# Kernel tuning notes

Hardware: AMD Instinct MI355X
Metric: run time of the kernel (lower is better)

## Reference

```python
import jax, jax.numpy as jnp
import numpy as np

EPS = 1e-12  # matches torch F.normalize eps


def _gradients(img):
    # forward differences along D, H, W with last slice zeroed (via zero-pad)
    dx = jnp.pad(img[:, :, 1:] - img[:, :, :-1], ((0, 0), (0, 0), (0, 1), (0, 0), (0, 0)))
    dy = jnp.pad(img[:, :, :, 1:] - img[:, :, :, :-1], ((0, 0), (0, 0), (0, 0), (0, 1), (0, 0)))
    dz = jnp.pad(img[:, :, :, :, 1:] - img[:, :, :, :, :-1], ((0, 0), (0, 0), (0, 0), (0, 0), (0, 1)))
    return dx, dy, dz


def _cos(f, t, axis):
    # cosine similarity along `axis` with torch-normalize eps semantics
    fn = f / jnp.maximum(jnp.linalg.norm(f, axis=axis, keepdims=True), EPS)
    tn = t / jnp.maximum(jnp.linalg.norm(t, axis=axis, keepdims=True), EPS)
    return jnp.sum(fn * tn, axis=axis)


def _sploss(f, t, ax_row, ax_col):
    # trace(norm_rows(F) @ norm_rows(T)^T) == sum of row cosine sims; same for cols.
    bc = f.shape[0] * f.shape[1]
    a = jnp.sum(_cos(f, t, ax_col)) / (f.shape[ax_row] * bc)
    b = jnp.sum(_cos(f, t, ax_row)) / (f.shape[ax_col] * bc)
    return -(a + b)


def setup_inputs() -> dict:
    key = jax.random.key(0)
    k1, k2 = jax.random.split(key)
    shape = (2, 1, 160, 160, 160)  # [B, C, D, H, W]
    fake = jax.random.normal(k1, shape, dtype=jnp.float32)
    true = jax.random.normal(k2, shape, dtype=jnp.float32)
    return {"fake": fake, "true": true}


def reference(fake, true):
    fx, fy, fz = _gradients(fake)
    tx, ty, tz = _gradients(true)
    # dim='x' slices are [H, W] -> rows axis 3, cols axis 4
    trace_x = _sploss(fx, tx, 3, 4)
    # dim='y' slices are [D, W] -> rows axis 2, cols axis 4
    trace_y = _sploss(fy, ty, 2, 4)
    # dim='z' slices are [D, H] -> rows axis 2, cols axis 3
    trace_z = _sploss(fz, tz, 2, 3)
    return (trace_x + trace_y + trace_z) / 3.0
```

## Files before the change

kernel.cpp:

```cpp
#include <hip/hip_runtime.h>
#include <math.h>

#define DD 160
#define HH 160
#define WW 160
#define NB 2
#define SLICE (HH * WW)
#define NV 51200
#define Dt 4
#define NDC 40
#define NHC 10
#define HCS 16
#define NTHR 320

static constexpr float EPS = 1e-12f;
static constexpr float SCALE = -1.0f / 960.0f;

#define ELEM(v, j) ((j) == 0 ? (v).x : ((j) == 1 ? (v).y : ((j) == 2 ? (v).z : (v).w)))

__global__ void zero_kernel(float* out) {
  if (threadIdx.x == 0) out[0] = 0.0f;
}

__global__ __launch_bounds__(NTHR, 2) void mainS(const float* __restrict__ f,
                                                 const float* __restrict__ t,
                                                 float* __restrict__ P,
                                                 float* __restrict__ out) {
  __shared__ float sw[HCS * 40 * 7];
  __shared__ float sh[8 * 40 * 25];
  __shared__ float red[HCS][6];
  __shared__ float cpad[HCS];
  const int tid = threadIdx.x;
  const int g = tid / 40;
  const int l = tid % 40;
  const int w = 4 * l;
  const int wn = (w + 4 < WW) ? (w + 4) : (WW - 1);
  const int hc = blockIdx.x % NHC;
  const int t2 = blockIdx.x / NHC;
  const int dc = t2 % NDC;
  const int b  = t2 / NDC;
  const int d0 = dc * Dt;
  const int r0 = hc * HCS + g * 2;
  const int r1 = r0 + 1;
  const int r2 = (r1 + 1 < HH) ? (r1 + 1) : (HH - 1);
  const float* fb = f + (size_t)b * DD * SLICE;
  const float* tb = t + (size_t)b * DD * SLICE;
  float* pH = P;
  float* pD = P + (size_t)NHC * 6 * NV;

  float4 S0f = *(const float4*)(fb + (size_t)d0 * SLICE + r0 * WW + w);
  float4 S0t = *(const float4*)(tb + (size_t)d0 * SLICE + r0 * WW + w);
  float4 S1f = *(const float4*)(fb + (size_t)d0 * SLICE + r1 * WW + w);
  float4 S1t = *(const float4*)(tb + (size_t)d0 * SLICE + r1 * WW + w);
  float s0fz = (fb + (size_t)d0 * SLICE + r0 * WW)[wn];
  float s0tz = (tb + (size_t)d0 * SLICE + r0 * WW)[wn];
  float s1fz = (fb + (size_t)d0 * SLICE + r1 * WW)[wn];
  float s1tz = (tb + (size_t)d0 * SLICE + r1 * WW)[wn];

  float aD[48];
#pragma unroll
  for (int c = 0; c < 48; ++c) aD[c] = 0.0f;
  float accCos = 0.0f;

#pragma unroll
  for (int p = 0; p < Dt; ++p) {
    const int d = d0 + p;
    const int dn = (d + 1 < DD) ? (d + 1) : d;
    const float* fS = fb + (size_t)d * SLICE;
    const float* tS = tb + (size_t)d * SLICE;
    const float* fN = fb + (size_t)dn * SLICE;
    const float* tN = tb + (size_t)dn * SLICE;
    const float4 Hf  = *(const float4*)(fS + r2 * WW + w);
    const float4 Ht  = *(const float4*)(tS + r2 * WW + w);
    const float4 D0f = *(const float4*)(fN + r0 * WW + w);
    const float4 D0t = *(const float4*)(tN + r0 * WW + w);
    const float4 D1f = *(const float4*)(fN + r1 * WW + w);
    const float4 D1t = *(const float4*)(tN + r1 * WW + w);
    const float d0fz = (fN + r0 * WW)[wn], d0tz = (tN + r0 * WW)[wn];
    const float d1fz = (fN + r1 * WW)[wn], d1tz = (tN + r1 * WW)[wn];

    float aH[24];
#pragma unroll
    for (int c = 0; c < 24; ++c) aH[c] = 0.0f;

    {
      float xd = 0, xf = 0, xt = 0, yd = 0, yf = 0, yt = 0;
#pragma unroll
      for (int j = 0; j < 4; ++j) {
        const float f0 = ELEM(S0f, j), t0 = ELEM(S0t, j);
        const float gxf = ELEM(D0f, j) - f0, gxt = ELEM(D0t, j) - t0;
        const float gyf = ELEM(S1f, j) - f0, gyt = ELEM(S1t, j) - t0;
        const float fnx = (j < 3) ? ELEM(S0f, j + 1) : s0fz;
        const float tnx = (j < 3) ? ELEM(S0t, j + 1) : s0tz;
        const float gzf = fnx - f0, gzt = tnx - t0;
        xd += gxf * gxt; xf += gxf * gxf; xt += gxt * gxt;
        yd += gyf * gyt; yf += gyf * gyf; yt += gyt * gyt;
        aH[j * 6 + 0] += gxf * gxt; aH[j * 6 + 1] += gxf * gxf; aH[j * 6 + 2] += gxt * gxt;
        aH[j * 6 + 3] += gzf * gzt; aH[j * 6 + 4] += gzf * gzf; aH[j * 6 + 5] += gzt * gzt;
        aD[j * 6 + 0] += gyf * gyt; aD[j * 6 + 1] += gyf * gyf; aD[j * 6 + 2] += gyt * gyt;
        aD[j * 6 + 3] += gzf * gzt; aD[j * 6 + 4] += gzf * gzf; aD[j * 6 + 5] += gzt * gzt;
      }
      float* s = &sw[((g * 2 + 0) * 40 + l) * 7];
      s[0] = xd; s[1] = xf; s[2] = xt; s[3] = yd; s[4] = yf; s[5] = yt;
    }
    {
      float xd = 0, xf = 0, xt = 0, yd = 0, yf = 0, yt = 0;
#pragma unroll
      for (int j = 0; j < 4; ++j) {
        const float f0 = ELEM(S1f, j), t0 = ELEM(S1t, j);
        const float gxf = ELEM(D1f, j) - f0, gxt = ELEM(D1t, j) - t0;
        const float gyf = ELEM(Hf, j) - f0, gyt = ELEM(Ht, j) - t0;
        const float fnx = (j < 3) ? ELEM(S1f, j + 1) : s1fz;
        const float tnx = (j < 3) ? ELEM(S1t, j + 1) : s1tz;
        const float gzf = fnx - f0, gzt = tnx - t0;
        xd += gxf * gxt; xf += gxf * gxf; xt += gxt * gxt;
        yd += gyf * gyt; yf += gyf * gyf; yt += gyt * gyt;
        aH[j * 6 + 0] += gxf * gxt; aH[j * 6 + 1] += gxf * gxf; aH[j * 6 + 2] += gxt * gxt;
        aH[j * 6 + 3] += gzf * gzt; aH[j * 6 + 4] += gzf * gzf; aH[j * 6 + 5] += gzt * gzt;
        aD[(4 + j) * 6 + 0] += gyf * gyt; aD[(4 + j) * 6 + 1] += gyf * gyf; aD[(4 + j) * 6 + 2] += gyt * gyt;
        aD[(4 + j) * 6 + 3] += gzf * gzt; aD[(4 + j) * 6 + 4] += gzf * gzf; aD[(4 + j) * 6 + 5] += gzt * gzt;
      }
      float* s = &sw[((g * 2 + 1) * 40 + l) * 7];
      s[0] = xd; s[1] = xf; s[2] = xt; s[3] = yd; s[4] = yf; s[5] = yt;
    }
    {
      float* s2 = &sh[(g * 40 + l) * 25];
#pragma unroll
      for (int c = 0; c < 24; ++c) s2[c] = aH[c];
    }
    S0f = D0f; S0t = D0t; S1f = D1f; S1t = D1t;
    s0fz = d0fz; s0tz = d0tz; s1fz = d1fz; s1tz = d1tz;
    __syncthreads();

    if (tid < 240) {
      const int cc = tid / 40, ll = tid % 40;
      float v0 = 0, v1 = 0, v2 = 0, v3 = 0;
#pragma unroll
      for (int gg = 0; gg < 8; ++gg) {
        const float* q = &sh[(gg * 40 + ll) * 25];
        v0 += q[0 * 6 + cc]; v1 += q[1 * 6 + cc]; v2 += q[2 * 6 + cc]; v3 += q[3 * 6 + cc];
      }
      const int bd = b * DD + d;
      float4 o; o.x = v0; o.y = v1; o.z = v2; o.w = v3;
      *(float4*)(pH + ((size_t)(hc * 6 + cc)) * NV + bd * 160 + 4 * ll) = o;
    } else {
      for (int k = tid - 240; k < HCS * 6; k += 80) {
        const int row = k / 6, c = k % 6;
        float s = 0.0f;
#pragma unroll 8
        for (int ll = 0; ll < 40; ++ll) s += sw[(row * 40 + ll) * 7 + c];
        red[row][c] = s;
      }
    }
    __syncthreads();
    if (tid < HCS) {
      const float cx = red[tid][0] / (fmaxf(sqrtf(red[tid][1]), EPS) * fmaxf(sqrtf(red[tid][2]), EPS));
      const float cy = red[tid][3] / (fmaxf(sqrtf(red[tid][4]), EPS) * fmaxf(sqrtf(red[tid][5]), EPS));
      accCos += cx + cy;
    }
  }

#pragma unroll
  for (int r = 0; r < 2; ++r) {
    const int h = r0 + r;
#pragma unroll
    for (int cc = 0; cc < 6; ++cc) {
      float4 o;
      o.x = aD[(r * 4 + 0) * 6 + cc];
      o.y = aD[(r * 4 + 1) * 6 + cc];
      o.z = aD[(r * 4 + 2) * 6 + cc];
      o.w = aD[(r * 4 + 3) * 6 + cc];
      *(float4*)(pD + ((size_t)(dc * 6 + cc)) * NV + b * SLICE + h * 160 + 4 * l) = o;
    }
  }

  if (tid < HCS) cpad[tid] = accCos;
  __syncthreads();
  if (tid == 0) {
    float s = 0.0f;
#pragma unroll
    for (int i = 0; i < HCS; ++i) s += cpad[i];
    atomicAdd(out, s * SCALE);
  }
}

__global__ __launch_bounds__(256) void finalize_kernel(const float* __restrict__ P,
                                                       float* __restrict__ out) {
  const int v = blockIdx.x * 256 + threadIdx.x;
  float c = 0.0f;
  if (v < 4 * NV) {
    const int type = v / NV;
    const int vec = v % NV;
    float dot = 0.0f, ff = 0.0f, tt = 0.0f;
    if (type < 2) {
#pragma unroll
      for (int ch = 0; ch < NHC; ++ch) {
        const float* q = P + ((size_t)(ch * 6 + type * 3)) * NV + vec;
        dot += q[0]; ff += q[(size_t)NV]; tt += q[2 * (size_t)NV];
      }
    } else {
      const float* pD = P + (size_t)NHC * 6 * NV;
#pragma unroll 8
      for (int ch = 0; ch < NDC; ++ch) {
        const float* q = pD + ((size_t)(ch * 6 + (type - 2) * 3)) * NV + vec;
        dot += q[0]; ff += q[(size_t)NV]; tt += q[2 * (size_t)NV];
      }
    }
    c = dot / (fmaxf(sqrtf(ff), EPS) * fmaxf(sqrtf(tt), EPS));
  }
#pragma unroll
  for (int m = 32; m >= 1; m >>= 1) c += __shfl_xor(c, m);
  __shared__ float part[4];
  if ((threadIdx.x & 63) == 0) part[threadIdx.x >> 6] = c;
  __syncthreads();
  if (threadIdx.x == 0) atomicAdd(out, (part[0] + part[1] + part[2] + part[3]) * SCALE);
}

extern "C" void kernel_launch(void* const* d_in, const int* in_sizes, int n_in,
                              void* d_out, int out_size, void* d_ws, size_t ws_size,
                              hipStream_t stream) {
  const float* fk = (const float*)d_in[0];
  const float* tr = (const float*)d_in[1];
  float* out = (float*)d_out;
  float* P = (float*)d_ws;

  hipLaunchKernelGGL(zero_kernel, dim3(1), dim3(64), 0, stream, out);
  hipLaunchKernelGGL(mainS, dim3(NB * NDC * NHC), dim3(NTHR), 0, stream, fk, tr, P, out);
  hipLaunchKernelGGL(finalize_kernel, dim3((4 * NV + 255) / 256), dim3(256), 0, stream, P, out);
}
```

Baseline: 145.8 us.

## Split D-axis partial sums into separate kernel to shrink partial buffer

Moves the per-(b,h,w) D-direction partial accumulation out of the main kernel into a new gradD kernel that sums over D in only four chunks. The partial buffer for the y/z cosines therefore drops from 40 chunks to 4, which cuts the workspace writes and the finalize reads. It also software-prefetches the next D slice in the main kernel. The cost is a second full read of both inputs and an extra kernel launch.

```diff
diff --git a/kernel.cpp b/kernel.cpp
--- a/kernel.cpp
+++ b/kernel.cpp
@@ -12,6 +12,8 @@
 #define NHC 10
 #define HCS 16
 #define NTHR 320
+#define DQ 4
+#define DPG 5
 
 static constexpr float EPS = 1e-12f;
 static constexpr float SCALE = -1.0f / 960.0f;
@@ -22,9 +24,9 @@
   if (threadIdx.x == 0) out[0] = 0.0f;
 }
 
-__global__ __launch_bounds__(NTHR, 2) void mainS(const float* __restrict__ f,
+__global__ __launch_bounds__(NTHR, 2) void gradH(const float* __restrict__ f,
                                                  const float* __restrict__ t,
-                                                 float* __restrict__ P,
+                                                 float* __restrict__ pH,
                                                  float* __restrict__ out) {
   __shared__ float sw[HCS * 40 * 7];
   __shared__ float sh[8 * 40 * 25];
@@ -45,8 +47,6 @@
   const int r2 = (r1 + 1 < HH) ? (r1 + 1) : (HH - 1);
   const float* fb = f + (size_t)b * DD * SLICE;
   const float* tb = t + (size_t)b * DD * SLICE;
-  float* pH = P;
-  float* pD = P + (size_t)NHC * 6 * NV;
 
   float4 S0f = *(const float4*)(fb + (size_t)d0 * SLICE + r0 * WW + w);
   float4 S0t = *(const float4*)(tb + (size_t)d0 * SLICE + r0 * WW + w);
@@ -56,28 +56,39 @@
   float s0tz = (tb + (size_t)d0 * SLICE + r0 * WW)[wn];
   float s1fz = (fb + (size_t)d0 * SLICE + r1 * WW)[wn];
   float s1tz = (tb + (size_t)d0 * SLICE + r1 * WW)[wn];
-
-  float aD[48];
-#pragma unroll
-  for (int c = 0; c < 48; ++c) aD[c] = 0.0f;
+  const float* fN0 = fb + (size_t)(d0 + 1) * SLICE;
+  const float* tN0 = tb + (size_t)(d0 + 1) * SLICE;
+  float4 D0f = *(const float4*)(fN0 + r0 * WW + w);
+  float4 D0t = *(const float4*)(tN0 + r0 * WW + w);
+  float4 D1f = *(const float4*)(fN0 + r1 * WW + w);
+  float4 D1t = *(const float4*)(tN0 + r1 * WW + w);
+  float d0fz = (fN0 + r0 * WW)[wn], d0tz = (tN0 + r0 * WW)[wn];
+  float d1fz = (fN0 + r1 * WW)[wn], d1tz = (tN0 + r1 * WW)[wn];
+
   float accCos = 0.0f;
 
 #pragma unroll
   for (int p = 0; p < Dt; ++p) {
     const int d = d0 + p;
-    const int dn = (d + 1 < DD) ? (d + 1) : d;
     const float* fS = fb + (size_t)d * SLICE;
     const float* tS = tb + (size_t)d * SLICE;
-    const float* fN = fb + (size_t)dn * SLICE;
-    const float* tN = tb + (size_t)dn * SLICE;
-    const float4 Hf  = *(const float4*)(fS + r2 * WW + w);
-    const float4 Ht  = *(const float4*)(tS + r2 * WW + w);
-    const float4 D0f = *(const float4*)(fN + r0 * WW + w);
-    const float4 D0t = *(const float4*)(tN + r0 * WW + w);
-    const float4 D1f = *(const float4*)(fN + r1 * WW + w);
-    const float4 D1t = *(const float4*)(tN + r1 * WW + w);
-    const float d0fz = (fN + r0 * WW)[wn], d0tz = (tN + r0 * WW)[wn];
-    const float d1fz = (fN + r1 * WW)[wn], d1tz = (tN + r1 * WW)[wn];
+    const float4 Hf = *(const float4*)(fS + r2 * WW + w);
+    const float4 Ht = *(const float4*)(tS + r2 * WW + w);
+    float4 nD0f = {0, 0, 0, 0}, nD0t = {0, 0, 0, 0};
+    float4 nD1f = {0, 0, 0, 0}, nD1t = {0, 0, 0, 0};
+    float n0fz = 0.f, n0tz = 0.f, n1fz = 0.f, n1tz = 0.f;
+    if (p < Dt - 1) {
+      const int nd = d + 1;
+      const int ndn = (nd + 1 < DD) ? (nd + 1) : nd;
+      const float* fN = fb + (size_t)ndn * SLICE;
+      const float* tN = tb + (size_t)ndn * SLICE;
+      nD0f = *(const float4*)(fN + r0 * WW + w);
+      nD0t = *(const float4*)(tN + r0 * WW + w);
+      nD1f = *(const float4*)(fN + r1 * WW + w);
+      nD1t = *(const float4*)(tN + r1 * WW + w);
+      n0fz = (fN + r0 * WW)[wn]; n0tz = (tN + r0 * WW)[wn];
+      n1fz = (fN + r1 * WW)[wn]; n1tz = (tN + r1 * WW)[wn];
+    }
 
     float aH[24];
 #pragma unroll
@@ -97,8 +108,6 @@
         yd += gyf * gyt; yf += gyf * gyf; yt += gyt * gyt;
         aH[j * 6 + 0] += gxf * gxt; aH[j * 6 + 1] += gxf * gxf; aH[j * 6 + 2] += gxt * gxt;
         aH[j * 6 + 3] += gzf * gzt; aH[j * 6 + 4] += gzf * gzf; aH[j * 6 + 5] += gzt * gzt;
-        aD[j * 6 + 0] += gyf * gyt; aD[j * 6 + 1] += gyf * gyf; aD[j * 6 + 2] += gyt * gyt;
-        aD[j * 6 + 3] += gzf * gzt; aD[j * 6 + 4] += gzf * gzf; aD[j * 6 + 5] += gzt * gzt;
       }
       float* s = &sw[((g * 2 + 0) * 40 + l) * 7];
       s[0] = xd; s[1] = xf; s[2] = xt; s[3] = yd; s[4] = yf; s[5] = yt;
@@ -117,8 +126,6 @@
         yd += gyf * gyt; yf += gyf * gyf; yt += gyt * gyt;
         aH[j * 6 + 0] += gxf * gxt; aH[j * 6 + 1] += gxf * gxf; aH[j * 6 + 2] += gxt * gxt;
         aH[j * 6 + 3] += gzf * gzt; aH[j * 6 + 4] += gzf * gzf; aH[j * 6 + 5] += gzt * gzt;
-        aD[(4 + j) * 6 + 0] += gyf * gyt; aD[(4 + j) * 6 + 1] += gyf * gyf; aD[(4 + j) * 6 + 2] += gyt * gyt;
-        aD[(4 + j) * 6 + 3] += gzf * gzt; aD[(4 + j) * 6 + 4] += gzf * gzf; aD[(4 + j) * 6 + 5] += gzt * gzt;
       }
       float* s = &sw[((g * 2 + 1) * 40 + l) * 7];
       s[0] = xd; s[1] = xf; s[2] = xt; s[3] = yd; s[4] = yf; s[5] = yt;
@@ -130,6 +137,10 @@
     }
     S0f = D0f; S0t = D0t; S1f = D1f; S1t = D1t;
     s0fz = d0fz; s0tz = d0tz; s1fz = d1fz; s1tz = d1tz;
+    if (p < Dt - 1) {
+      D0f = nD0f; D0t = nD0t; D1f = nD1f; D1t = nD1t;
+      d0fz = n0fz; d0tz = n0tz; d1fz = n1fz; d1tz = n1tz;
+    }
     __syncthreads();
 
     if (tid < 240) {
@@ -160,20 +171,6 @@
     }
   }
 
-#pragma unroll
-  for (int r = 0; r < 2; ++r) {
-    const int h = r0 + r;
-#pragma unroll
-    for (int cc = 0; cc < 6; ++cc) {
-      float4 o;
-      o.x = aD[(r * 4 + 0) * 6 + cc];
-      o.y = aD[(r * 4 + 1) * 6 + cc];
-      o.z = aD[(r * 4 + 2) * 6 + cc];
-      o.w = aD[(r * 4 + 3) * 6 + cc];
-      *(float4*)(pD + ((size_t)(dc * 6 + cc)) * NV + b * SLICE + h * 160 + 4 * l) = o;
-    }
-  }
-
   if (tid < HCS) cpad[tid] = accCos;
   __syncthreads();
   if (tid == 0) {
@@ -184,7 +181,71 @@
   }
 }
 
-__global__ __launch_bounds__(256) void finalize_kernel(const float* __restrict__ P,
+__global__ __launch_bounds__(NTHR, 2) void gradD(const float* __restrict__ f,
+                                                 const float* __restrict__ t,
+                                                 float* __restrict__ pD) {
+  __shared__ float sh[8 * 40 * 25];
+  const int tid = threadIdx.x;
+  const int g = tid / 40;
+  const int l = tid % 40;
+  const int w = 4 * l;
+  const int wn = (w + 4 < WW) ? (w + 4) : (WW - 1);
+  const int dq = blockIdx.x % DQ;
+  const int t2 = blockIdx.x / DQ;
+  const int h = t2 % HH;
+  const int b = t2 / HH;
+  const int hn = (h + 1 < HH) ? (h + 1) : h;
+  const float* rowF  = f + (size_t)b * DD * SLICE + h * WW;
+  const float* rowT  = t + (size_t)b * DD * SLICE + h * WW;
+  const float* rowFn = f + (size_t)b * DD * SLICE + hn * WW;
+  const float* rowTn = t + (size_t)b * DD * SLICE + hn * WW;
+  const int dbeg = dq * (DD / DQ) + g * DPG;
+
+  float a[24];
+#pragma unroll
+  for (int c = 0; c < 24; ++c) a[c] = 0.0f;
+
+#pragma unroll
+  for (int i = 0; i < DPG; ++i) {
+    const size_t off = (size_t)(dbeg + i) * SLICE;
+    const float4 Sf = *(const float4*)(rowF + off + w);
+    const float4 St = *(const float4*)(rowT + off + w);
+    const float4 Nf = *(const float4*)(rowFn + off + w);
+    const float4 Nt = *(const float4*)(rowTn + off + w);
+    const float sfz = (rowF + off)[wn];
+    const float stz = (rowT + off)[wn];
+#pragma unroll
+    for (int j = 0; j < 4; ++j) {
+      const float f0 = ELEM(Sf, j), t0 = ELEM(St, j);
+      const float gyf = ELEM(Nf, j) - f0, gyt = ELEM(Nt, j) - t0;
+      const float fnx = (j < 3) ? ELEM(Sf, j + 1) : sfz;
+      const float tnx = (j < 3) ? ELEM(St, j + 1) : stz;
+      const float gzf = fnx - f0, gzt = tnx - t0;
+      a[j * 6 + 0] += gyf * gyt; a[j * 6 + 1] += gyf * gyf; a[j * 6 + 2] += gyt * gyt;
+      a[j * 6 + 3] += gzf * gzt; a[j * 6 + 4] += gzf * gzf; a[j * 6 + 5] += gzt * gzt;
+    }
+  }
+  {
+    float* s2 = &sh[(g * 40 + l) * 25];
+#pragma unroll
+    for (int c = 0; c < 24; ++c) s2[c] = a[c];
+  }
+  __syncthreads();
+  if (tid < 240) {
+    const int cc = tid / 40, ll = tid % 40;
+    float v0 = 0, v1 = 0, v2 = 0, v3 = 0;
+#pragma unroll
+    for (int gg = 0; gg < 8; ++gg) {
+      const float* q = &sh[(gg * 40 + ll) * 25];
+      v0 += q[0 * 6 + cc]; v1 += q[1 * 6 + cc]; v2 += q[2 * 6 + cc]; v3 += q[3 * 6 + cc];
+    }
+    float4 o; o.x = v0; o.y = v1; o.z = v2; o.w = v3;
+    *(float4*)(pD + ((size_t)(dq * 6 + cc)) * NV + b * SLICE + h * 160 + 4 * ll) = o;
+  }
+}
+
+__global__ __launch_bounds__(256) void finalize_kernel(const float* __restrict__ PH,
+                                                       const float* __restrict__ PD,
                                                        float* __restrict__ out) {
   const int v = blockIdx.x * 256 + threadIdx.x;
   float c = 0.0f;
@@ -193,16 +254,17 @@
     const int vec = v % NV;
     float dot = 0.0f, ff = 0.0f, tt = 0.0f;
     if (type < 2) {
+      const float* base = PH + (size_t)(type * 3) * NV + vec;
 #pragma unroll
       for (int ch = 0; ch < NHC; ++ch) {
-        const float* q = P + ((size_t)(ch * 6 + type * 3)) * NV + vec;
+        const float* q = base + (size_t)(ch * 6) * NV;
         dot += q[0]; ff += q[(size_t)NV]; tt += q[2 * (size_t)NV];
       }
     } else {
-      const float* pD = P + (size_t)NHC * 6 * NV;
-#pragma unroll 8
-      for (int ch = 0; ch < NDC; ++ch) {
-        const float* q = pD + ((size_t)(ch * 6 + (type - 2) * 3)) * NV + vec;
+      const float* base = PD + (size_t)((type - 2) * 3) * NV + vec;
+#pragma unroll
+      for (int ch = 0; ch < DQ; ++ch) {
+        const float* q = base + (size_t)(ch * 6) * NV;
         dot += q[0]; ff += q[(size_t)NV]; tt += q[2 * (size_t)NV];
       }
     }
@@ -222,9 +284,11 @@
   const float* fk = (const float*)d_in[0];
   const float* tr = (const float*)d_in[1];
   float* out = (float*)d_out;
-  float* P = (float*)d_ws;
+  float* PH = (float*)d_ws;
+  float* PD = PH + (size_t)NHC * 6 * NV;
 
   hipLaunchKernelGGL(zero_kernel, dim3(1), dim3(64), 0, stream, out);
-  hipLaunchKernelGGL(mainS, dim3(NB * NDC * NHC), dim3(NTHR), 0, stream, fk, tr, P, out);
-  hipLaunchKernelGGL(finalize_kernel, dim3((4 * NV + 255) / 256), dim3(256), 0, stream, P, out);
-}
+  hipLaunchKernelGGL(gradH, dim3(NB * NDC * NHC), dim3(NTHR), 0, stream, fk, tr, PH, out);
+  hipLaunchKernelGGL(gradD, dim3(NB * HH * DQ), dim3(NTHR), 0, stream, fk, tr, PD);
+  hipLaunchKernelGGL(finalize_kernel, dim3((4 * NV + 255) / 256), dim3(256), 0, stream, PH, PD, out);
+}
```

Result: slower. 158.5 us (+8.7%).

## Accumulate D-direction partials with atomics and prefetch next depth slice

Applied to the files above, without the earlier changes.

The per-depth-chunk partial buffer (40 chunks × 6 channels) is replaced by a single 6-channel buffer. A new zeroing kernel clears it, and each block adds into it with atomicAdd, so finalize reads one value instead of summing 40 chunk partials. The main loop also software-prefetches the next slice's D-neighbour rows one iteration ahead to overlap loads with compute. The cost is atomic contention (40 adders per address) and scalar atomics in place of float4 stores. It also makes float summation order nondeterministic.

```diff
diff --git a/kernel.cpp b/kernel.cpp
--- a/kernel.cpp
+++ b/kernel.cpp
@@ -18,14 +18,18 @@
 
 #define ELEM(v, j) ((j) == 0 ? (v).x : ((j) == 1 ? (v).y : ((j) == 2 ? (v).z : (v).w)))
 
-__global__ void zero_kernel(float* out) {
-  if (threadIdx.x == 0) out[0] = 0.0f;
-}
-
-__global__ __launch_bounds__(NTHR, 2) void mainS(const float* __restrict__ f,
-                                                 const float* __restrict__ t,
-                                                 float* __restrict__ P,
-                                                 float* __restrict__ out) {
+__global__ __launch_bounds__(256) void zeroP(float4* __restrict__ pD4,
+                                             float* __restrict__ out) {
+  const int i = blockIdx.x * 256 + threadIdx.x;
+  pD4[i] = make_float4(0.0f, 0.0f, 0.0f, 0.0f);
+  if (i == 0) out[0] = 0.0f;
+}
+
+__global__ __launch_bounds__(NTHR, 2) void mainS2(const float* __restrict__ f,
+                                                  const float* __restrict__ t,
+                                                  float* __restrict__ pH,
+                                                  float* __restrict__ pD2,
+                                                  float* __restrict__ out) {
   __shared__ float sw[HCS * 40 * 7];
   __shared__ float sh[8 * 40 * 25];
   __shared__ float red[HCS][6];
@@ -45,8 +49,6 @@
   const int r2 = (r1 + 1 < HH) ? (r1 + 1) : (HH - 1);
   const float* fb = f + (size_t)b * DD * SLICE;
   const float* tb = t + (size_t)b * DD * SLICE;
-  float* pH = P;
-  float* pD = P + (size_t)NHC * 6 * NV;
 
   float4 S0f = *(const float4*)(fb + (size_t)d0 * SLICE + r0 * WW + w);
   float4 S0t = *(const float4*)(tb + (size_t)d0 * SLICE + r0 * WW + w);
@@ -56,6 +58,14 @@
   float s0tz = (tb + (size_t)d0 * SLICE + r0 * WW)[wn];
   float s1fz = (fb + (size_t)d0 * SLICE + r1 * WW)[wn];
   float s1tz = (tb + (size_t)d0 * SLICE + r1 * WW)[wn];
+  const float* fN0 = fb + (size_t)(d0 + 1) * SLICE;
+  const float* tN0 = tb + (size_t)(d0 + 1) * SLICE;
+  float4 D0f = *(const float4*)(fN0 + r0 * WW + w);
+  float4 D0t = *(const float4*)(tN0 + r0 * WW + w);
+  float4 D1f = *(const float4*)(fN0 + r1 * WW + w);
+  float4 D1t = *(const float4*)(tN0 + r1 * WW + w);
+  float d0fz = (fN0 + r0 * WW)[wn], d0tz = (tN0 + r0 * WW)[wn];
+  float d1fz = (fN0 + r1 * WW)[wn], d1tz = (tN0 + r1 * WW)[wn];
 
   float aD[48];
 #pragma unroll
@@ -65,19 +75,25 @@
 #pragma unroll
   for (int p = 0; p < Dt; ++p) {
     const int d = d0 + p;
-    const int dn = (d + 1 < DD) ? (d + 1) : d;
     const float* fS = fb + (size_t)d * SLICE;
     const float* tS = tb + (size_t)d * SLICE;
-    const float* fN = fb + (size_t)dn * SLICE;
-    const float* tN = tb + (size_t)dn * SLICE;
-    const float4 Hf  = *(const float4*)(fS + r2 * WW + w);
-    const float4 Ht  = *(const float4*)(tS + r2 * WW + w);
-    const float4 D0f = *(const float4*)(fN + r0 * WW + w);
-    const float4 D0t = *(const float4*)(tN + r0 * WW + w);
-    const float4 D1f = *(const float4*)(fN + r1 * WW + w);
-    const float4 D1t = *(const float4*)(tN + r1 * WW + w);
-    const float d0fz = (fN + r0 * WW)[wn], d0tz = (tN + r0 * WW)[wn];
-    const float d1fz = (fN + r1 * WW)[wn], d1tz = (tN + r1 * WW)[wn];
+    const float4 Hf = *(const float4*)(fS + r2 * WW + w);
+    const float4 Ht = *(const float4*)(tS + r2 * WW + w);
+    float4 nD0f = {0, 0, 0, 0}, nD0t = {0, 0, 0, 0};
+    float4 nD1f = {0, 0, 0, 0}, nD1t = {0, 0, 0, 0};
+    float n0fz = 0.f, n0tz = 0.f, n1fz = 0.f, n1tz = 0.f;
+    if (p < Dt - 1) {
+      const int nd = d + 1;
+      const int ndn = (nd + 1 < DD) ? (nd + 1) : nd;
+      const float* fN = fb + (size_t)ndn * SLICE;
+      const float* tN = tb + (size_t)ndn * SLICE;
+      nD0f = *(const float4*)(fN + r0 * WW + w);
+      nD0t = *(const float4*)(tN + r0 * WW + w);
+      nD1f = *(const float4*)(fN + r1 * WW + w);
+      nD1t = *(const float4*)(tN + r1 * WW + w);
+      n0fz = (fN + r0 * WW)[wn]; n0tz = (tN + r0 * WW)[wn];
+      n1fz = (fN + r1 * WW)[wn]; n1tz = (tN + r1 * WW)[wn];
+    }
 
     float aH[24];
 #pragma unroll
@@ -130,6 +146,10 @@
     }
     S0f = D0f; S0t = D0t; S1f = D1f; S1t = D1t;
     s0fz = d0fz; s0tz = d0tz; s1fz = d1fz; s1tz = d1tz;
+    if (p < Dt - 1) {
+      D0f = nD0f; D0t = nD0t; D1f = nD1f; D1t = nD1t;
+      d0fz = n0fz; d0tz = n0tz; d1fz = n1fz; d1tz = n1tz;
+    }
     __syncthreads();
 
     if (tid < 240) {
@@ -165,12 +185,10 @@
     const int h = r0 + r;
 #pragma unroll
     for (int cc = 0; cc < 6; ++cc) {
-      float4 o;
-      o.x = aD[(r * 4 + 0) * 6 + cc];
-      o.y = aD[(r * 4 + 1) * 6 + cc];
-      o.z = aD[(r * 4 + 2) * 6 + cc];
-      o.w = aD[(r * 4 + 3) * 6 + cc];
-      *(float4*)(pD + ((size_t)(dc * 6 + cc)) * NV + b * SLICE + h * 160 + 4 * l) = o;
+      float* base = pD2 + (size_t)cc * NV + b * SLICE + h * 160 + 4 * l;
+#pragma unroll
+      for (int j = 0; j < 4; ++j)
+        atomicAdd(base + j, aD[(r * 4 + j) * 6 + cc]);
     }
   }
 
@@ -184,7 +202,8 @@
   }
 }
 
-__global__ __launch_bounds__(256) void finalize_kernel(const float* __restrict__ P,
+__global__ __launch_bounds__(256) void finalize_kernel(const float* __restrict__ PH,
+                                                       const float* __restrict__ PD2,
                                                        float* __restrict__ out) {
   const int v = blockIdx.x * 256 + threadIdx.x;
   float c = 0.0f;
@@ -193,18 +212,15 @@
     const int vec = v % NV;
     float dot = 0.0f, ff = 0.0f, tt = 0.0f;
     if (type < 2) {
+      const float* base = PH + (size_t)(type * 3) * NV + vec;
 #pragma unroll
       for (int ch = 0; ch < NHC; ++ch) {
-        const float* q = P + ((size_t)(ch * 6 + type * 3)) * NV + vec;
+        const float* q = base + (size_t)(ch * 6) * NV;
         dot += q[0]; ff += q[(size_t)NV]; tt += q[2 * (size_t)NV];
       }
     } else {
-      const float* pD = P + (size_t)NHC * 6 * NV;
-#pragma unroll 8
-      for (int ch = 0; ch < NDC; ++ch) {
-        const float* q = pD + ((size_t)(ch * 6 + (type - 2) * 3)) * NV + vec;
-        dot += q[0]; ff += q[(size_t)NV]; tt += q[2 * (size_t)NV];
-      }
+      const float* q = PD2 + (size_t)((type - 2) * 3) * NV + vec;
+      dot = q[0]; ff = q[(size_t)NV]; tt = q[2 * (size_t)NV];
     }
     c = dot / (fmaxf(sqrtf(ff), EPS) * fmaxf(sqrtf(tt), EPS));
   }
@@ -222,9 +238,13 @@
   const float* fk = (const float*)d_in[0];
   const float* tr = (const float*)d_in[1];
   float* out = (float*)d_out;
-  float* P = (float*)d_ws;
-
-  hipLaunchKernelGGL(zero_kernel, dim3(1), dim3(64), 0, stream, out);
-  hipLaunchKernelGGL(mainS, dim3(NB * NDC * NHC), dim3(NTHR), 0, stream, fk, tr, P, out);
-  hipLaunchKernelGGL(finalize_kernel, dim3((4 * NV + 255) / 256), dim3(256), 0, stream, P, out);
-}
+  float* PH  = (float*)d_ws;
+  float* PD2 = PH + (size_t)NHC * 6 * NV;
+
+  hipLaunchKernelGGL(zeroP, dim3(6 * NV / 4 / 256), dim3(256), 0, stream,
+                     (float4*)PD2, out);
+  hipLaunchKernelGGL(mainS2, dim3(NB * NDC * NHC), dim3(NTHR), 0, stream,
+                     fk, tr, PH, PD2, out);
+  hipLaunchKernelGGL(finalize_kernel, dim3((4 * NV + 255) / 256), dim3(256), 0, stream,
+                     PH, PD2, out);
+}
```

Result: slower. 293.5 us (+101.3%).
